# Performance work log

Hardware: AMD Instinct MI355X
Metric: run time of the kernel (lower is better)

## Reference

```python
import jax, jax.numpy as jnp
import numpy as np

D_MODEL = 32
D_STATE = 16
D_CONV = 4
D_INNER = 64  # expand * d_model
DT_RANK = 2   # ceil(d_model / 16)


def silu(x):
    return x * jax.nn.sigmoid(x)


def _mamba_params(key, scale=0.05):
    ks = jax.random.split(key, 7)
    p = {}
    p['in_w'] = jax.random.normal(ks[0], (2 * D_INNER, D_MODEL), jnp.float32) * scale
    p['conv_w'] = jax.random.normal(ks[1], (D_INNER, 1, D_CONV), jnp.float32) * scale
    p['conv_b'] = jax.random.normal(ks[2], (D_INNER,), jnp.float32) * scale
    p['xproj_w'] = jax.random.normal(ks[3], (DT_RANK + 2 * D_STATE, D_INNER), jnp.float32) * scale
    p['dt_w'] = jax.random.normal(ks[4], (D_INNER, DT_RANK), jnp.float32) * scale
    p['dt_b'] = jax.random.normal(ks[5], (D_INNER,), jnp.float32) * scale
    # S4D-real init: A = [1..d_state] broadcast over d_inner
    p['A_log'] = jnp.log(jnp.broadcast_to(jnp.arange(1, D_STATE + 1, dtype=jnp.float32), (D_INNER, D_STATE)))
    p['D'] = jnp.ones((D_INNER,), jnp.float32)
    p['out_w'] = jax.random.normal(ks[6], (D_MODEL, D_INNER), jnp.float32) * scale
    return p


def mamba(x, in_w, conv_w, conv_b, xproj_w, dt_w, dt_b, A_log, Dp, out_w):
    # x: (B, L, d_model)
    Bsz, L, _ = x.shape
    xz = x @ in_w.T                                   # (B, L, 2*d_inner)
    xi, z = jnp.split(xz, 2, axis=-1)
    # causal depthwise conv over L
    xc = jnp.pad(xi.transpose(0, 2, 1), ((0, 0), (0, 0), (D_CONV - 1, 0)))  # (B, d_inner, L+3)
    xc = jax.lax.conv_general_dilated(xc, conv_w, (1,), 'VALID',
                                      dimension_numbers=('NCH', 'OIH', 'NCH'),
                                      feature_group_count=D_INNER)
    xi = silu(xc.transpose(0, 2, 1) + conv_b)          # (B, L, d_inner)
    dbc = xi @ xproj_w.T                               # (B, L, dt_rank + 2*d_state)
    dt = dbc[..., :DT_RANK]
    Bm = dbc[..., DT_RANK:DT_RANK + D_STATE]           # (B, L, d_state)
    Cm = dbc[..., DT_RANK + D_STATE:]                  # (B, L, d_state)
    delta = jax.nn.softplus(dt @ dt_w.T + dt_b)        # (B, L, d_inner)
    A = -jnp.exp(A_log)                                # (d_inner, d_state)
    deltaA = jnp.exp(delta[..., None] * A)             # (B, L, d_inner, d_state)
    deltaBx = delta[..., None] * Bm[:, :, None, :] * xi[..., None]

    def step(h, t):
        dA, dBx = t
        h = dA * h + dBx
        return h, h

    h0 = jnp.zeros((Bsz, D_INNER, D_STATE), x.dtype)
    _, hs = jax.lax.scan(step, h0, (deltaA.transpose(1, 0, 2, 3), deltaBx.transpose(1, 0, 2, 3)))
    hs = hs.transpose(1, 0, 2, 3)                      # (B, L, d_inner, d_state)
    y = jnp.einsum('blds,bls->bld', hs, Cm) + Dp * xi
    y = y * silu(z)
    return y @ out_w.T                                 # (B, L, d_model)


def setup_inputs() -> dict:
    key = jax.random.key(0)
    ks = jax.random.split(key, 12)
    s = 0.05
    inp = {'inputs': jax.random.normal(ks[0], (32, 512, 64, 64), jnp.float32)}
    inp['proj_avg_w'] = jax.random.normal(ks[1], (D_MODEL, 1), jnp.float32) * s
    inp['proj_avg_b'] = jax.random.normal(ks[2], (D_MODEL,), jnp.float32) * s
    inp['proj_max_w'] = jax.random.normal(ks[3], (D_MODEL, 1), jnp.float32) * s
    inp['proj_max_b'] = jax.random.normal(ks[4], (D_MODEL,), jnp.float32) * s
    inp['gate_w'] = jax.random.normal(ks[5], (1, 2), jnp.float32) * s
    inp['gate_b'] = jax.random.normal(ks[6], (1,), jnp.float32) * s
    inp['out_w'] = jax.random.normal(ks[7], (1, D_MODEL), jnp.float32) * s
    inp['out_b'] = jax.random.normal(ks[8], (1,), jnp.float32) * s
    pf = _mamba_params(ks[9])
    pb = _mamba_params(ks[10])
    for k, v in pf.items():
        inp['f_' + k] = v
    for k, v in pb.items():
        inp['b_' + k] = v
    return inp


def reference(inputs, proj_avg_w, proj_avg_b, proj_max_w, proj_max_b, gate_w, gate_b,
              out_w, out_b,
              f_in_w, f_conv_w, f_conv_b, f_xproj_w, f_dt_w, f_dt_b, f_A_log, f_D, f_out_w,
              b_in_w, b_conv_w, b_conv_b, b_xproj_w, b_dt_w, b_dt_b, b_A_log, b_D, b_out_w):
    # global avg / max pool -> (B, C, 1)
    x_avg = jnp.mean(inputs, axis=(2, 3))[..., None]
    x_max = jnp.max(inputs, axis=(2, 3))[..., None]
    gate_in = jnp.concatenate([x_avg, x_max], axis=-1)            # (B, C, 2)
    alpha = jax.nn.sigmoid(gate_in @ gate_w.T + gate_b)           # (B, C, 1)
    xa = x_avg @ proj_avg_w.T + proj_avg_b                        # (B, C, d_model)
    xm = x_max @ proj_max_w.T + proj_max_b
    fwd = (f_in_w, f_conv_w, f_conv_b, f_xproj_w, f_dt_w, f_dt_b, f_A_log, f_D, f_out_w)
    bwd = (b_in_w, b_conv_w, b_conv_b, b_xproj_w, b_dt_w, b_dt_b, b_A_log, b_D, b_out_w)
    y_avg = mamba(xa, *fwd) + jnp.flip(mamba(jnp.flip(xa, 1), *bwd), 1)
    y_max = mamba(xm, *fwd) + jnp.flip(mamba(jnp.flip(xm, 1), *bwd), 1)
    y = alpha * y_avg + (1.0 - alpha) * y_max
    att = jax.nn.sigmoid(y @ out_w.T + out_b)                     # (B, C, 1)
    return att[..., None]                                         # (B, C, 1, 1)
```

## Files before the change

### kernel.cpp

```cpp
#include <hip/hip_runtime.h>
#include <math.h>

#define OFF_YPART 32768
#define OFF_PD    294912
#define OFF_PX    (OFF_PD + 4194304)
#define OFF_PG    (OFF_PX + 4194304)
#define OFF_BCB   (OFF_PG + 4194304)
#define OFF_BCC   (OFF_BCB + 524288)
#define OFF_YB    (OFF_BCC + 524288)
#define OFF_CONST (OFF_YB + 65536)

__global__ __launch_bounds__(256) void kreduce(const float* __restrict__ in,
                                               float* __restrict__ xavg,
                                               float* __restrict__ xmax) {
    const int bl = blockIdx.x;
    const float* p = in + (size_t)bl * 4096;
    const int t = threadIdx.x;
    float s = 0.f, m = -INFINITY;
#pragma unroll
    for (int it = 0; it < 4; ++it) {
        float4 v = *reinterpret_cast<const float4*>(p + (size_t)(it * 256 + t) * 4);
        s += v.x + v.y + v.z + v.w;
        m = fmaxf(m, fmaxf(fmaxf(v.x, v.y), fmaxf(v.z, v.w)));
    }
#pragma unroll
    for (int o = 1; o < 64; o <<= 1) {
        s += __shfl_xor(s, o);
        m = fmaxf(m, __shfl_xor(m, o));
    }
    __shared__ float ls[4], lm[4];
    const int w = t >> 6;
    if ((t & 63) == 0) { ls[w] = s; lm[w] = m; }
    __syncthreads();
    if (t == 0) {
        s = ls[0] + ls[1] + ls[2] + ls[3];
        m = fmaxf(fmaxf(lm[0], lm[1]), fmaxf(lm[2], lm[3]));
        xavg[bl] = s * (1.f / 4096.f);
        xmax[bl] = m;
    }
}

__global__ __launch_bounds__(128) void kconst(
    float* __restrict__ ws,
    const float* __restrict__ paw, const float* __restrict__ pab,
    const float* __restrict__ pmw, const float* __restrict__ pmb,
    const float* __restrict__ outw_outer,
    const float* __restrict__ f_in_w, const float* __restrict__ f_out_w,
    const float* __restrict__ b_in_w, const float* __restrict__ b_out_w)
{
    const int c = blockIdx.x;
    const int t = threadIdx.x;
    const int strm = c >> 1, dir = c & 1;
    const float* in_w = dir ? b_in_w : f_in_w;
    const float* owp  = dir ? b_out_w : f_out_w;
    const float* projw = strm ? pmw : paw;
    const float* projb = strm ? pmb : pab;

    float u = 0.f, v = 0.f;
    const float* row = in_w + t * 32;
#pragma unroll
    for (int m = 0; m < 32; ++m) {
        u = fmaf(row[m], projw[m], u);
        v = fmaf(row[m], projb[m], v);
    }
    ws[OFF_CONST + c * 320 + t] = u;
    ws[OFF_CONST + c * 320 + 128 + t] = v;
    if (t < 64) {
        float wf = 0.f;
#pragma unroll
        for (int m = 0; m < 32; ++m) wf = fmaf(outw_outer[m], owp[m * 64 + t], wf);
        ws[OFF_CONST + c * 320 + 256 + t] = wf;
    }
}

__device__ __forceinline__ int dbc_slot(int j) {
    return j < 2 ? j : (j < 18 ? 2 * j - 2 : 2 * j - 33);
}

__global__ __launch_bounds__(512, 4) void kprep(
    const float* __restrict__ xavg, const float* __restrict__ xmax,
    float* __restrict__ ws,
    const float* __restrict__ f_conv_w, const float* __restrict__ f_conv_b,
    const float* __restrict__ f_xproj_w, const float* __restrict__ f_dt_w,
    const float* __restrict__ f_dt_b, const float* __restrict__ f_D,
    const float* __restrict__ b_conv_w, const float* __restrict__ b_conv_b,
    const float* __restrict__ b_xproj_w, const float* __restrict__ b_dt_w,
    const float* __restrict__ b_dt_b, const float* __restrict__ b_D)
{
    const int tid = threadIdx.x;
    const int c  = blockIdx.x >> 8;
    const int b  = (blockIdx.x >> 3) & 31;
    const int cq = blockIdx.x & 7;
    const int strm = c >> 1, dir = c & 1;

    const float* cwp  = dir ? b_conv_w : f_conv_w;
    const float* cbp  = dir ? b_conv_b : f_conv_b;
    const float* xpw  = dir ? b_xproj_w: f_xproj_w;
    const float* dtwp = dir ? b_dt_w   : f_dt_w;
    const float* dtbp = dir ? b_dt_b   : f_dt_b;
    const float* Dpar = dir ? b_D      : f_D;
    const float* xin  = strm ? xmax : xavg;

    __shared__ float sseq4[68];
    __shared__ float su[128], sv[128];
    __shared__ float scw[64][4], scb[64], sdtw[64][2], sdtb[64], sD[64], swf[64];
    __shared__ float sxp[34][68];
    __shared__ float sxi[64][68];
    __shared__ float sdbc[64][37];

    if (tid < 67) {
        int g = cq * 64 - 3 + tid;
        float val = 0.f;
        if (g >= 0) val = xin[b * 512 + (dir ? (511 - g) : g)];
        sseq4[tid] = val;
    }
    if (tid < 128) {
        su[tid] = ws[OFF_CONST + c * 320 + tid];
        sv[tid] = ws[OFF_CONST + c * 320 + 128 + tid];
    }
    if (tid < 64) {
#pragma unroll
        for (int k = 0; k < 4; ++k) scw[tid][k] = cwp[tid * 4 + k];
        scb[tid] = cbp[tid];
        sdtw[tid][0] = dtwp[tid * 2];
        sdtw[tid][1] = dtwp[tid * 2 + 1];
        sdtb[tid] = dtbp[tid];
        sD[tid] = Dpar[tid];
        swf[tid] = ws[OFF_CONST + c * 320 + 256 + tid];
    }
    for (int i = tid; i < 34 * 64; i += 512) sxp[i >> 6][i & 63] = xpw[i];
    __syncthreads();

    const int ll8 = tid >> 3;
    const int j8  = tid & 7;
    const int gi  = cq * 64 + ll8;

    {
        float t0 = sseq4[ll8], t1 = sseq4[ll8 + 1], t2 = sseq4[ll8 + 2], t3 = sseq4[ll8 + 3];
        float vv0 = (gi >= 3) ? 1.f : 0.f;
        float vv1 = (gi >= 2) ? 1.f : 0.f;
        float vv2 = (gi >= 1) ? 1.f : 0.f;
#pragma unroll
        for (int k = 0; k < 8; ++k) {
            int di = j8 * 8 + k;
            float u = su[di], v = sv[di];
            float xc = scw[di][0] * fmaf(t0, u, vv0 * v)
                     + scw[di][1] * fmaf(t1, u, vv1 * v)
                     + scw[di][2] * fmaf(t2, u, vv2 * v)
                     + scw[di][3] * fmaf(t3, u, v);
            xc += scb[di];
            float sig = 1.f / (1.f + __expf(-xc));
            sxi[ll8][di] = xc * sig;
        }
    }
    __syncthreads();

    {
        float a0 = 0.f, a1 = 0.f, a2 = 0.f, a3 = 0.f, a4 = 0.f;
        const float4* xr4 = reinterpret_cast<const float4*>(&sxi[ll8][0]);
        const float4* r0 = reinterpret_cast<const float4*>(&sxp[j8 + 0][0]);
        const float4* r1 = reinterpret_cast<const float4*>(&sxp[j8 + 8][0]);
        const float4* r2 = reinterpret_cast<const float4*>(&sxp[j8 + 16][0]);
        const float4* r3 = reinterpret_cast<const float4*>(&sxp[j8 + 24][0]);
        const float4* r4 = (j8 < 2) ? reinterpret_cast<const float4*>(&sxp[j8 + 32][0]) : r0;
        bool extra = (j8 < 2);
#pragma unroll 2
        for (int q = 0; q < 16; ++q) {
            float4 x = xr4[q];
            float4 w;
            w = r0[q]; a0 = fmaf(x.x,w.x,fmaf(x.y,w.y,fmaf(x.z,w.z,fmaf(x.w,w.w,a0))));
            w = r1[q]; a1 = fmaf(x.x,w.x,fmaf(x.y,w.y,fmaf(x.z,w.z,fmaf(x.w,w.w,a1))));
            w = r2[q]; a2 = fmaf(x.x,w.x,fmaf(x.y,w.y,fmaf(x.z,w.z,fmaf(x.w,w.w,a2))));
            w = r3[q]; a3 = fmaf(x.x,w.x,fmaf(x.y,w.y,fmaf(x.z,w.z,fmaf(x.w,w.w,a3))));
            if (extra) { w = r4[q]; a4 = fmaf(x.x,w.x,fmaf(x.y,w.y,fmaf(x.z,w.z,fmaf(x.w,w.w,a4)))); }
        }
        sdbc[ll8][dbc_slot(j8)]      = a0;
        sdbc[ll8][dbc_slot(j8 + 8)]  = a1;
        sdbc[ll8][dbc_slot(j8 + 16)] = a2;
        sdbc[ll8][dbc_slot(j8 + 24)] = a3;
        if (extra) sdbc[ll8][dbc_slot(j8 + 32)] = a4;
    }
    __syncthreads();

    {
        const size_t tile = ((size_t)(c * 32 + b) * 8 + cq) * 4096;
        float dt0 = sdbc[ll8][0], dt1 = sdbc[ll8][1];
        float x3 = sseq4[ll8 + 3];
        float ybp = 0.f;
        float pdv[8], pxv[8], pgv[8];
#pragma unroll
        for (int k = 0; k < 8; ++k) {
            int di = j8 * 8 + k;
            float xi = sxi[ll8][di];
            float pre = fmaf(dt0, sdtw[di][0], fmaf(dt1, sdtw[di][1], sdtb[di]));
            float sp = (pre > 20.f) ? pre : log1pf(__expf(pre));
            float zv = fmaf(x3, su[64 + di], sv[64 + di]);
            float g = (zv / (1.f + __expf(-zv))) * swf[di];
            pdv[k] = sp;
            pxv[k] = sp * xi;
            pgv[k] = g;
            ybp = fmaf(g * sD[di], xi, ybp);
        }
        float* bp = ws + OFF_PD + tile + ll8 * 64 + j8 * 8;
        *reinterpret_cast<float4*>(bp)     = float4{pdv[0], pdv[1], pdv[2], pdv[3]};
        *reinterpret_cast<float4*>(bp + 4) = float4{pdv[4], pdv[5], pdv[6], pdv[7]};
        bp = ws + OFF_PX + tile + ll8 * 64 + j8 * 8;
        *reinterpret_cast<float4*>(bp)     = float4{pxv[0], pxv[1], pxv[2], pxv[3]};
        *reinterpret_cast<float4*>(bp + 4) = float4{pxv[4], pxv[5], pxv[6], pxv[7]};
        bp = ws + OFF_PG + tile + ll8 * 64 + j8 * 8;
        *reinterpret_cast<float4*>(bp)     = float4{pgv[0], pgv[1], pgv[2], pgv[3]};
        *reinterpret_cast<float4*>(bp + 4) = float4{pgv[4], pgv[5], pgv[6], pgv[7]};
        ybp += __shfl_xor(ybp, 1);
        ybp += __shfl_xor(ybp, 2);
        ybp += __shfl_xor(ybp, 4);
        if (j8 == 0) ws[OFF_YB + (size_t)(c * 32 + b) * 512 + gi] = ybp;
    }

    {
        const size_t bb = ((size_t)(c * 32 + b) * 8 + cq) * 1024;
        for (int i = tid; i < 1024; i += 512) {
            int s = i >> 6, t = i & 63;
            ws[OFF_BCB + bb + i] = sdbc[t][2 + 2 * s];
            ws[OFF_BCC + bb + i] = sdbc[t][3 + 2 * s];
        }
    }
}

#define DPP_ADD(v, ctrl) ((v) + __int_as_float(__builtin_amdgcn_update_dpp(0, __float_as_int(v), (ctrl), 0xF, 0xF, true)))

__global__ __launch_bounds__(256, 4) void kscan(
    float* __restrict__ ws,
    const float* __restrict__ f_A_log, const float* __restrict__ b_A_log)
{
    const int tid = threadIdx.x;
    const int c  = blockIdx.x >> 7;
    const int dq = (blockIdx.x >> 5) & 3;
    const int b  = blockIdx.x & 31;
    const int dir = c & 1;
    const float* alog = dir ? b_A_log : f_A_log;

    const int dd = tid >> 4;
    const int s  = tid & 15;
    const int d  = dq * 16 + dd;
    const float cA = -expf(alog[d * 16 + s]) * 1.44269504088896340736f;
    float h = 0.f;

    __shared__ float sd[16][68], sx[16][68], sg[16][68];
    __shared__ float sB[16][68], sC[16][68];
    __shared__ float syT[16][68];
    __shared__ float syb[64];

    const int srow = tid >> 4;
    const int scol = (tid & 15) * 4;
    const int st = tid >> 2;
    const int sc = (tid & 3) * 4;
    float* ypart = ws + OFF_YPART;

    for (int chunk = 0; chunk < 8; ++chunk) {
        const size_t tb = (size_t)(c * 32 + b) * 8 + chunk;
        const float* pd = ws + OFF_PD + tb * 4096;
        const float* px = ws + OFF_PX + tb * 4096;
        const float* pg = ws + OFF_PG + tb * 4096;
        const float* pB = ws + OFF_BCB + tb * 1024;
        const float* pC = ws + OFF_BCC + tb * 1024;

        {
            float4 vd = *reinterpret_cast<const float4*>(pd + st * 64 + dq * 16 + sc);
            float4 vx = *reinterpret_cast<const float4*>(px + st * 64 + dq * 16 + sc);
            float4 vg = *reinterpret_cast<const float4*>(pg + st * 64 + dq * 16 + sc);
            sd[sc + 0][st] = vd.x; sd[sc + 1][st] = vd.y; sd[sc + 2][st] = vd.z; sd[sc + 3][st] = vd.w;
            sx[sc + 0][st] = vx.x; sx[sc + 1][st] = vx.y; sx[sc + 2][st] = vx.z; sx[sc + 3][st] = vx.w;
            sg[sc + 0][st] = vg.x; sg[sc + 1][st] = vg.y; sg[sc + 2][st] = vg.z; sg[sc + 3][st] = vg.w;
            *reinterpret_cast<float4*>(&sB[srow][scol]) =
                *reinterpret_cast<const float4*>(pB + srow * 64 + scol);
            *reinterpret_cast<float4*>(&sC[srow][scol]) =
                *reinterpret_cast<const float4*>(pC + srow * 64 + scol);
            if (dq == 0 && tid < 64) syb[tid] = ws[OFF_YB + (size_t)(c * 32 + b) * 512 + chunk * 64 + tid];
        }
        __syncthreads();

        {
#pragma unroll 2
            for (int m = 0; m < 16; ++m) {
                float4 de = *reinterpret_cast<const float4*>(&sd[dd][4 * m]);
                float4 dx = *reinterpret_cast<const float4*>(&sx[dd][4 * m]);
                float4 gq = *reinterpret_cast<const float4*>(&sg[dd][4 * m]);
                float4 Bq = *reinterpret_cast<const float4*>(&sB[s][4 * m]);
                float4 Cq = *reinterpret_cast<const float4*>(&sC[s][4 * m]);
                float4 val;
                float a, pc;
                a = exp2f(de.x * cA); h = fmaf(a, h, dx.x * Bq.x); pc = h * Cq.x;
                pc = DPP_ADD(pc, 0x101); pc = DPP_ADD(pc, 0x102);
                pc = DPP_ADD(pc, 0x104); pc = DPP_ADD(pc, 0x108);
                val.x = pc * gq.x;
                a = exp2f(de.y * cA); h = fmaf(a, h, dx.y * Bq.y); pc = h * Cq.y;
                pc = DPP_ADD(pc, 0x101); pc = DPP_ADD(pc, 0x102);
                pc = DPP_ADD(pc, 0x104); pc = DPP_ADD(pc, 0x108);
                val.y = pc * gq.y;
                a = exp2f(de.z * cA); h = fmaf(a, h, dx.z * Bq.z); pc = h * Cq.z;
                pc = DPP_ADD(pc, 0x101); pc = DPP_ADD(pc, 0x102);
                pc = DPP_ADD(pc, 0x104); pc = DPP_ADD(pc, 0x108);
                val.z = pc * gq.z;
                a = exp2f(de.w * cA); h = fmaf(a, h, dx.w * Bq.w); pc = h * Cq.w;
                pc = DPP_ADD(pc, 0x101); pc = DPP_ADD(pc, 0x102);
                pc = DPP_ADD(pc, 0x104); pc = DPP_ADD(pc, 0x108);
                val.w = pc * gq.w;
                if (s == 0) *reinterpret_cast<float4*>(&syT[dd][4 * m]) = val;
            }
        }
        __syncthreads();

        {
            const int tt4 = tid >> 2;
            const int j4  = tid & 3;
            float acc = syT[j4 * 4][tt4] + syT[j4 * 4 + 1][tt4]
                      + syT[j4 * 4 + 2][tt4] + syT[j4 * 4 + 3][tt4];
            acc += __shfl_xor(acc, 1);
            acc += __shfl_xor(acc, 2);
            if (j4 == 0) {
                int i = chunk * 64 + tt4;
                int l = dir ? (511 - i) : i;
                float res = acc + (dq == 0 ? syb[tt4] : 0.f);
                ypart[((c * 4 + dq) * 32 + b) * 512 + l] = res;
            }
        }
        __syncthreads();
    }
}

__global__ __launch_bounds__(256) void kfinal(const float* __restrict__ xavg,
                                              const float* __restrict__ xmax,
                                              const float* __restrict__ ypart,
                                              const float* __restrict__ gate_w,
                                              const float* __restrict__ gate_b,
                                              const float* __restrict__ out_b,
                                              float* __restrict__ out) {
    const int idx = blockIdx.x * 256 + threadIdx.x;
    float xa = xavg[idx], xm = xmax[idx];
    float alpha = 1.f / (1.f + __expf(-(fmaf(xa, gate_w[0], fmaf(xm, gate_w[1], gate_b[0])))));
    float sa = 0.f, sm = 0.f;
#pragma unroll
    for (int k = 0; k < 8; ++k)  sa += ypart[k * 16384 + idx];
#pragma unroll
    for (int k = 8; k < 16; ++k) sm += ypart[k * 16384 + idx];
    float y = alpha * sa + (1.f - alpha) * sm + out_b[0];
    out[idx] = 1.f / (1.f + __expf(-y));
}

extern "C" void kernel_launch(void* const* d_in, const int* in_sizes, int n_in,
                              void* d_out, int out_size, void* d_ws, size_t ws_size,
                              hipStream_t stream) {
    const float* inp = (const float*)d_in[0];
    const float* paw = (const float*)d_in[1];
    const float* pab = (const float*)d_in[2];
    const float* pmw = (const float*)d_in[3];
    const float* pmb = (const float*)d_in[4];
    const float* gw  = (const float*)d_in[5];
    const float* gb  = (const float*)d_in[6];
    const float* ow  = (const float*)d_in[7];
    const float* ob  = (const float*)d_in[8];

    float* ws = (float*)d_ws;
    float* xavg = ws;
    float* xmax = ws + 16384;
    float* ypart = ws + OFF_YPART;
    float* out = (float*)d_out;

    kconst<<<4, 128, 0, stream>>>(
        ws, paw, pab, pmw, pmb, ow,
        (const float*)d_in[9], (const float*)d_in[17],
        (const float*)d_in[18], (const float*)d_in[26]);
    kreduce<<<16384, 256, 0, stream>>>(inp, xavg, xmax);
    kprep<<<1024, 512, 0, stream>>>(
        xavg, xmax, ws,
        (const float*)d_in[10], (const float*)d_in[11], (const float*)d_in[12],
        (const float*)d_in[13], (const float*)d_in[14], (const float*)d_in[16],
        (const float*)d_in[19], (const float*)d_in[20], (const float*)d_in[21],
        (const float*)d_in[22], (const float*)d_in[23], (const float*)d_in[25]);
    kscan<<<512, 256, 0, stream>>>(
        ws, (const float*)d_in[15], (const float*)d_in[24]);
    kfinal<<<64, 256, 0, stream>>>(xavg, xmax, ypart, gw, gb, ob, out);
}
```

Baseline: 133.8 us.

## Split sequential chunk scan into parallel two-pass chunked scan with carry combine

Replaces the single scan kernel, which walked 8 chunks in sequence per block, with three kernels. A first sweep computes each chunk's end state from zero and its cumulative decay. A combine kernel propagates carries across chunks, and a second sweep reruns each chunk from its incoming state to produce outputs. This gives 8x more blocks to fill the GPU, at the cost of roughly doubling the exp and recurrence work, adding two kernel launches, and adding extra global traffic for the intermediate states.

```diff
diff --git a/kernel.cpp b/kernel.cpp
--- a/kernel.cpp
+++ b/kernel.cpp
@@ -9,6 +9,9 @@
 #define OFF_BCC   (OFF_BCB + 524288)
 #define OFF_YB    (OFF_BCC + 524288)
 #define OFF_CONST (OFF_YB + 65536)
+#define OFF_HE    (OFF_CONST + 2048)
+#define OFF_AP    (OFF_HE + 1048576)
+#define OFF_HIN   (OFF_AP + 1048576)
 
 __global__ __launch_bounds__(256) void kreduce(const float* __restrict__ in,
                                                float* __restrict__ xavg,
@@ -228,14 +231,16 @@
 
 #define DPP_ADD(v, ctrl) ((v) + __int_as_float(__builtin_amdgcn_update_dpp(0, __float_as_int(v), (ctrl), 0xF, 0xF, true)))
 
-__global__ __launch_bounds__(256, 4) void kscan(
+__global__ __launch_bounds__(256, 4) void ksweep1(
     float* __restrict__ ws,
     const float* __restrict__ f_A_log, const float* __restrict__ b_A_log)
 {
     const int tid = threadIdx.x;
-    const int c  = blockIdx.x >> 7;
-    const int dq = (blockIdx.x >> 5) & 3;
-    const int b  = blockIdx.x & 31;
+    const int idx = blockIdx.x;
+    const int chunk = idx & 7;
+    const int b  = (idx >> 3) & 31;
+    const int dq = (idx >> 8) & 3;
+    const int c  = idx >> 10;
     const int dir = c & 1;
     const float* alog = dir ? b_A_log : f_A_log;
 
@@ -243,7 +248,91 @@
     const int s  = tid & 15;
     const int d  = dq * 16 + dd;
     const float cA = -expf(alog[d * 16 + s]) * 1.44269504088896340736f;
-    float h = 0.f;
+
+    __shared__ float sd[16][68], sx[16][68];
+
+    const int st = tid >> 2;
+    const int sc = (tid & 3) * 4;
+    const size_t tb = (size_t)(c * 32 + b) * 8 + chunk;
+    {
+        const float* pd = ws + OFF_PD + tb * 4096;
+        const float* px = ws + OFF_PX + tb * 4096;
+        float4 vd = *reinterpret_cast<const float4*>(pd + st * 64 + dq * 16 + sc);
+        float4 vx = *reinterpret_cast<const float4*>(px + st * 64 + dq * 16 + sc);
+        sd[sc + 0][st] = vd.x; sd[sc + 1][st] = vd.y; sd[sc + 2][st] = vd.z; sd[sc + 3][st] = vd.w;
+        sx[sc + 0][st] = vx.x; sx[sc + 1][st] = vx.y; sx[sc + 2][st] = vx.z; sx[sc + 3][st] = vx.w;
+    }
+    __syncthreads();
+
+    float h = 0.f, Sd = 0.f;
+#pragma unroll 4
+    for (int m = 0; m < 16; ++m) {
+        float4 de = *reinterpret_cast<const float4*>(&sd[dd][4 * m]);
+        float4 dx = *reinterpret_cast<const float4*>(&sx[dd][4 * m]);
+        float a;
+        a = exp2f(de.x * cA); h = fmaf(a, h, dx.x);
+        a = exp2f(de.y * cA); h = fmaf(a, h, dx.y);
+        a = exp2f(de.z * cA); h = fmaf(a, h, dx.z);
+        a = exp2f(de.w * cA); h = fmaf(a, h, dx.w);
+        Sd += de.x + de.y + de.z + de.w;
+    }
+    (void)h;
+    __shared__ float sB[16][68];
+    {
+        const float* pB = ws + OFF_BCB + tb * 1024;
+        const int srow = tid >> 4;
+        const int scol = (tid & 15) * 4;
+        *reinterpret_cast<float4*>(&sB[srow][scol]) =
+            *reinterpret_cast<const float4*>(pB + srow * 64 + scol);
+    }
+    __syncthreads();
+    h = 0.f;
+#pragma unroll 2
+    for (int m = 0; m < 16; ++m) {
+        float4 de = *reinterpret_cast<const float4*>(&sd[dd][4 * m]);
+        float4 dx = *reinterpret_cast<const float4*>(&sx[dd][4 * m]);
+        float4 Bq = *reinterpret_cast<const float4*>(&sB[s][4 * m]);
+        float a;
+        a = exp2f(de.x * cA); h = fmaf(a, h, dx.x * Bq.x);
+        a = exp2f(de.y * cA); h = fmaf(a, h, dx.y * Bq.y);
+        a = exp2f(de.z * cA); h = fmaf(a, h, dx.z * Bq.z);
+        a = exp2f(de.w * cA); h = fmaf(a, h, dx.w * Bq.w);
+    }
+    ws[OFF_HE + (size_t)idx * 256 + tid] = h;
+    ws[OFF_AP + (size_t)idx * 256 + tid] = exp2f(cA * Sd);
+}
+
+__global__ __launch_bounds__(256, 4) void kcomb(float* __restrict__ ws)
+{
+    const int tid = threadIdx.x;
+    const int base = blockIdx.x * 8;
+    float hin = 0.f;
+#pragma unroll
+    for (int k = 0; k < 8; ++k) {
+        ws[OFF_HIN + (size_t)(base + k) * 256 + tid] = hin;
+        float aP = ws[OFF_AP + (size_t)(base + k) * 256 + tid];
+        float hE = ws[OFF_HE + (size_t)(base + k) * 256 + tid];
+        hin = fmaf(aP, hin, hE);
+    }
+}
+
+__global__ __launch_bounds__(256, 4) void ksweep2(
+    float* __restrict__ ws,
+    const float* __restrict__ f_A_log, const float* __restrict__ b_A_log)
+{
+    const int tid = threadIdx.x;
+    const int idx = blockIdx.x;
+    const int chunk = idx & 7;
+    const int b  = (idx >> 3) & 31;
+    const int dq = (idx >> 8) & 3;
+    const int c  = idx >> 10;
+    const int dir = c & 1;
+    const float* alog = dir ? b_A_log : f_A_log;
+
+    const int dd = tid >> 4;
+    const int s  = tid & 15;
+    const int d  = dq * 16 + dd;
+    const float cA = -expf(alog[d * 16 + s]) * 1.44269504088896340736f;
 
     __shared__ float sd[16][68], sx[16][68], sg[16][68];
     __shared__ float sB[16][68], sC[16][68];
@@ -255,76 +344,73 @@
     const int st = tid >> 2;
     const int sc = (tid & 3) * 4;
     float* ypart = ws + OFF_YPART;
-
-    for (int chunk = 0; chunk < 8; ++chunk) {
-        const size_t tb = (size_t)(c * 32 + b) * 8 + chunk;
+    const size_t tb = (size_t)(c * 32 + b) * 8 + chunk;
+
+    {
         const float* pd = ws + OFF_PD + tb * 4096;
         const float* px = ws + OFF_PX + tb * 4096;
         const float* pg = ws + OFF_PG + tb * 4096;
         const float* pB = ws + OFF_BCB + tb * 1024;
         const float* pC = ws + OFF_BCC + tb * 1024;
-
-        {
-            float4 vd = *reinterpret_cast<const float4*>(pd + st * 64 + dq * 16 + sc);
-            float4 vx = *reinterpret_cast<const float4*>(px + st * 64 + dq * 16 + sc);
-            float4 vg = *reinterpret_cast<const float4*>(pg + st * 64 + dq * 16 + sc);
-            sd[sc + 0][st] = vd.x; sd[sc + 1][st] = vd.y; sd[sc + 2][st] = vd.z; sd[sc + 3][st] = vd.w;
-            sx[sc + 0][st] = vx.x; sx[sc + 1][st] = vx.y; sx[sc + 2][st] = vx.z; sx[sc + 3][st] = vx.w;
-            sg[sc + 0][st] = vg.x; sg[sc + 1][st] = vg.y; sg[sc + 2][st] = vg.z; sg[sc + 3][st] = vg.w;
-            *reinterpret_cast<float4*>(&sB[srow][scol]) =
-                *reinterpret_cast<const float4*>(pB + srow * 64 + scol);
-            *reinterpret_cast<float4*>(&sC[srow][scol]) =
-                *reinterpret_cast<const float4*>(pC + srow * 64 + scol);
-            if (dq == 0 && tid < 64) syb[tid] = ws[OFF_YB + (size_t)(c * 32 + b) * 512 + chunk * 64 + tid];
-        }
-        __syncthreads();
-
-        {
+        float4 vd = *reinterpret_cast<const float4*>(pd + st * 64 + dq * 16 + sc);
+        float4 vx = *reinterpret_cast<const float4*>(px + st * 64 + dq * 16 + sc);
+        float4 vg = *reinterpret_cast<const float4*>(pg + st * 64 + dq * 16 + sc);
+        sd[sc + 0][st] = vd.x; sd[sc + 1][st] = vd.y; sd[sc + 2][st] = vd.z; sd[sc + 3][st] = vd.w;
+        sx[sc + 0][st] = vx.x; sx[sc + 1][st] = vx.y; sx[sc + 2][st] = vx.z; sx[sc + 3][st] = vx.w;
+        sg[sc + 0][st] = vg.x; sg[sc + 1][st] = vg.y; sg[sc + 2][st] = vg.z; sg[sc + 3][st] = vg.w;
+        *reinterpret_cast<float4*>(&sB[srow][scol]) =
+            *reinterpret_cast<const float4*>(pB + srow * 64 + scol);
+        *reinterpret_cast<float4*>(&sC[srow][scol]) =
+            *reinterpret_cast<const float4*>(pC + srow * 64 + scol);
+        if (dq == 0 && tid < 64) syb[tid] = ws[OFF_YB + (size_t)(c * 32 + b) * 512 + chunk * 64 + tid];
+    }
+    float h = ws[OFF_HIN + (size_t)idx * 256 + tid];
+    __syncthreads();
+
+    {
 #pragma unroll 2
-            for (int m = 0; m < 16; ++m) {
-                float4 de = *reinterpret_cast<const float4*>(&sd[dd][4 * m]);
-                float4 dx = *reinterpret_cast<const float4*>(&sx[dd][4 * m]);
-                float4 gq = *reinterpret_cast<const float4*>(&sg[dd][4 * m]);
-                float4 Bq = *reinterpret_cast<const float4*>(&sB[s][4 * m]);
-                float4 Cq = *reinterpret_cast<const float4*>(&sC[s][4 * m]);
-                float4 val;
-                float a, pc;
-                a = exp2f(de.x * cA); h = fmaf(a, h, dx.x * Bq.x); pc = h * Cq.x;
-                pc = DPP_ADD(pc, 0x101); pc = DPP_ADD(pc, 0x102);
-                pc = DPP_ADD(pc, 0x104); pc = DPP_ADD(pc, 0x108);
-                val.x = pc * gq.x;
-                a = exp2f(de.y * cA); h = fmaf(a, h, dx.y * Bq.y); pc = h * Cq.y;
-                pc = DPP_ADD(pc, 0x101); pc = DPP_ADD(pc, 0x102);
-                pc = DPP_ADD(pc, 0x104); pc = DPP_ADD(pc, 0x108);
-                val.y = pc * gq.y;
-                a = exp2f(de.z * cA); h = fmaf(a, h, dx.z * Bq.z); pc = h * Cq.z;
-                pc = DPP_ADD(pc, 0x101); pc = DPP_ADD(pc, 0x102);
-                pc = DPP_ADD(pc, 0x104); pc = DPP_ADD(pc, 0x108);
-                val.z = pc * gq.z;
-                a = exp2f(de.w * cA); h = fmaf(a, h, dx.w * Bq.w); pc = h * Cq.w;
-                pc = DPP_ADD(pc, 0x101); pc = DPP_ADD(pc, 0x102);
-                pc = DPP_ADD(pc, 0x104); pc = DPP_ADD(pc, 0x108);
-                val.w = pc * gq.w;
-                if (s == 0) *reinterpret_cast<float4*>(&syT[dd][4 * m]) = val;
-            }
-        }
-        __syncthreads();
-
-        {
-            const int tt4 = tid >> 2;
-            const int j4  = tid & 3;
-            float acc = syT[j4 * 4][tt4] + syT[j4 * 4 + 1][tt4]
-                      + syT[j4 * 4 + 2][tt4] + syT[j4 * 4 + 3][tt4];
-            acc += __shfl_xor(acc, 1);
-            acc += __shfl_xor(acc, 2);
-            if (j4 == 0) {
-                int i = chunk * 64 + tt4;
-                int l = dir ? (511 - i) : i;
-                float res = acc + (dq == 0 ? syb[tt4] : 0.f);
-                ypart[((c * 4 + dq) * 32 + b) * 512 + l] = res;
-            }
-        }
-        __syncthreads();
+        for (int m = 0; m < 16; ++m) {
+            float4 de = *reinterpret_cast<const float4*>(&sd[dd][4 * m]);
+            float4 dx = *reinterpret_cast<const float4*>(&sx[dd][4 * m]);
+            float4 gq = *reinterpret_cast<const float4*>(&sg[dd][4 * m]);
+            float4 Bq = *reinterpret_cast<const float4*>(&sB[s][4 * m]);
+            float4 Cq = *reinterpret_cast<const float4*>(&sC[s][4 * m]);
+            float4 val;
+            float a, pc;
+            a = exp2f(de.x * cA); h = fmaf(a, h, dx.x * Bq.x); pc = h * Cq.x;
+            pc = DPP_ADD(pc, 0x101); pc = DPP_ADD(pc, 0x102);
+            pc = DPP_ADD(pc, 0x104); pc = DPP_ADD(pc, 0x108);
+            val.x = pc * gq.x;
+            a = exp2f(de.y * cA); h = fmaf(a, h, dx.y * Bq.y); pc = h * Cq.y;
+            pc = DPP_ADD(pc, 0x101); pc = DPP_ADD(pc, 0x102);
+            pc = DPP_ADD(pc, 0x104); pc = DPP_ADD(pc, 0x108);
+            val.y = pc * gq.y;
+            a = exp2f(de.z * cA); h = fmaf(a, h, dx.z * Bq.z); pc = h * Cq.z;
+            pc = DPP_ADD(pc, 0x101); pc = DPP_ADD(pc, 0x102);
+            pc = DPP_ADD(pc, 0x104); pc = DPP_ADD(pc, 0x108);
+            val.z = pc * gq.z;
+            a = exp2f(de.w * cA); h = fmaf(a, h, dx.w * Bq.w); pc = h * Cq.w;
+            pc = DPP_ADD(pc, 0x101); pc = DPP_ADD(pc, 0x102);
+            pc = DPP_ADD(pc, 0x104); pc = DPP_ADD(pc, 0x108);
+            val.w = pc * gq.w;
+            if (s == 0) *reinterpret_cast<float4*>(&syT[dd][4 * m]) = val;
+        }
+    }
+    __syncthreads();
+
+    {
+        const int tt4 = tid >> 2;
+        const int j4  = tid & 3;
+        float acc = syT[j4 * 4][tt4] + syT[j4 * 4 + 1][tt4]
+                  + syT[j4 * 4 + 2][tt4] + syT[j4 * 4 + 3][tt4];
+        acc += __shfl_xor(acc, 1);
+        acc += __shfl_xor(acc, 2);
+        if (j4 == 0) {
+            int i = chunk * 64 + tt4;
+            int l = dir ? (511 - i) : i;
+            float res = acc + (dq == 0 ? syb[tt4] : 0.f);
+            ypart[((c * 4 + dq) * 32 + b) * 512 + l] = res;
+        }
     }
 }
 
@@ -377,7 +463,10 @@
         (const float*)d_in[13], (const float*)d_in[14], (const float*)d_in[16],
         (const float*)d_in[19], (const float*)d_in[20], (const float*)d_in[21],
         (const float*)d_in[22], (const float*)d_in[23], (const float*)d_in[25]);
-    kscan<<<512, 256, 0, stream>>>(
+    ksweep1<<<4096, 256, 0, stream>>>(
+        ws, (const float*)d_in[15], (const float*)d_in[24]);
+    kcomb<<<512, 256, 0, stream>>>(ws);
+    ksweep2<<<4096, 256, 0, stream>>>(
         ws, (const float*)d_in[15], (const float*)d_in[24]);
     kfinal<<<64, 256, 0, stream>>>(xavg, xmax, ypart, gw, gb, ob, out);
 }
```

New measurement: 145.3 us. 8.6% more time.
